# Optimization experiments

Measured on AMD Instinct MI355X. Metric: run time of the kernel, lower is better.

The kernel has to match this reference:

```python
import jax, jax.numpy as jnp
import numpy as np

B, T, D, H, HS = 2, 256, 2048, 32, 64
LORA, DLORA, ST = 32, 64, 66  # maa lora rank, decay lora rank, state rows (2+HS)
EPS = 1e-5


def setup_inputs() -> dict:
    key = jax.random.key(0)
    ks = jax.random.split(key, 24)
    n = lambda k, sh, s=0.02: (jax.random.normal(k, sh, jnp.float32) * s)
    u = lambda k, sh: jax.random.uniform(k, sh, jnp.float32)
    return {
        "x": jax.random.normal(ks[0], (B, T, D), jnp.float32),
        "state": jax.random.normal(ks[1], (B, ST, D), jnp.float32) * 0.1,
        "ln1_w": jnp.ones((D,), jnp.float32),
        "ln1_b": jnp.zeros((D,), jnp.float32),
        "time_maa_x": u(ks[2], (D,)),
        "time_maa_w1": n(ks[3], (D, 5 * LORA)),
        "time_maa_w2": n(ks[4], (5, LORA, D)),
        "time_maa_k": u(ks[5], (D,)),
        "time_maa_w": u(ks[6], (D,)),
        "time_maa_v": u(ks[7], (D,)),
        "time_maa_r": u(ks[8], (D,)),
        "time_maa_g": u(ks[9], (D,)),
        "time_decay": n(ks[10], (D,), 0.5),
        "time_decay_w1": n(ks[11], (D, DLORA)),
        "time_decay_w2": n(ks[12], (DLORA, D)),
        "time_faaaa": n(ks[13], (H, HS, 1), 0.1),
        "receptance_weight": n(ks[14], (D, D)),
        "key_weight": n(ks[15], (D, D)),
        "value_weight": n(ks[16], (D, D)),
        "output_weight": n(ks[17], (D, D)),
        "gate_weight": n(ks[18], (D, D)),
        "lnx_w": jnp.ones((D,), jnp.float32),
        "lnx_b": jnp.zeros((D,), jnp.float32),
        "i": 0,
    }


def reference(x, state, ln1_w, ln1_b, time_maa_x, time_maa_w1, time_maa_w2,
              time_maa_k, time_maa_w, time_maa_v, time_maa_r, time_maa_g,
              time_decay, time_decay_w1, time_decay_w2, time_faaaa,
              receptance_weight, key_weight, value_weight, output_weight,
              gate_weight, lnx_w, lnx_b, i):
    # forward() early-returns time_mixing(ln1(x), state, i)
    mu = x.mean(-1, keepdims=True)
    var = ((x - mu) ** 2).mean(-1, keepdims=True)
    x = (x - mu) * jax.lax.rsqrt(var + EPS) * ln1_w + ln1_b

    i1 = (2 + HS) * i + 1
    # token shift: sx[t] = x[t-1] - x[t], with state row i1 as x[-1]
    sx = jnp.concatenate([state[:, i1][:, None] - x[:, :1], x[:, :-1] - x[:, 1:]], axis=1)

    xxx = x + sx * time_maa_x
    t5 = jnp.tanh(xxx @ time_maa_w1).reshape(B, T, 5, LORA)
    xxx5 = jnp.einsum('btfr,frd->btfd', t5, time_maa_w2)          # [B,T,5,D]
    maa = jnp.stack([time_maa_k, time_maa_w, time_maa_v, time_maa_r, time_maa_g])  # [5,D]
    x5 = x[:, :, None] + sx[:, :, None] * (maa + xxx5)            # [B,T,5,D]

    k = (x5[:, :, 0] @ key_weight.T).reshape(B, T, H, HS)
    w = jnp.exp(-jnp.exp(time_decay + jnp.tanh(x5[:, :, 1] @ time_decay_w1) @ time_decay_w2)).reshape(B, T, H, HS)
    v = (x5[:, :, 2] @ value_weight.T).reshape(B, T, H, HS)
    r = (x5[:, :, 3] @ receptance_weight.T).reshape(B, T, H, HS)
    g = jax.nn.silu(x5[:, :, 4] @ gate_weight.T)                  # [B,T,D]

    kv = jnp.einsum('bthi,bthj->bthij', k, v)                     # [B,T,H,HS,HS]
    prev0 = state[:, i1 + 1:i1 + 1 + HS].reshape(B, H, HS, HS)

    def step(prev, xs):
        kv_t, w_t = xs
        return kv_t + w_t[..., None] * prev, prev  # emit state BEFORE update

    _, state_s = jax.lax.scan(step, prev0,
                              (kv.transpose(1, 0, 2, 3, 4), w.transpose(1, 0, 2, 3)))
    state_s = state_s.transpose(1, 0, 2, 3, 4)                    # [B,T,H,HS,HS]

    wkv = time_faaaa * kv + state_s
    rwkv = jnp.einsum('bthj,bthjd->bthd', r, wkv)                 # [B,T,H,HS]

    # GroupNorm(num_groups=H) over each head's HS channels
    gm = rwkv.mean(-1, keepdims=True)
    gv = ((rwkv - gm) ** 2).mean(-1, keepdims=True)
    normed = (rwkv - gm) * jax.lax.rsqrt(gv + EPS)
    normed = normed * lnx_w.reshape(H, HS) + lnx_b.reshape(H, HS)
    normed = normed.reshape(B, T, D)

    return (normed * g) @ output_weight.T
```

## Files before the change

kernel.cpp:

```cpp
#include <hip/hip_runtime.h>
#include <hip/hip_bf16.h>

typedef unsigned short u16;
typedef __attribute__((ext_vector_type(4))) float f32x4;
typedef __attribute__((ext_vector_type(8))) short short8;
typedef __attribute__((ext_vector_type(4))) short bf16x4;

#define B_ 2
#define T_ 256
#define D_ 2048
#define H_ 32
#define HS_ 64
#define M_ 512
#define ST_ 66
#define EPS_ 1e-5f
#define NC_ 16
#define CL_ 16

__device__ __forceinline__ float bf2f(u16 u) {
    union { unsigned int i; float f; } c; c.i = ((unsigned int)u) << 16; return c.f;
}
__device__ __forceinline__ u16 f2bf(float f) {
    union { unsigned int i; float f; } c; c.f = f;
    unsigned int r = c.i + 0x7fffu + ((c.i >> 16) & 1u);
    return (u16)(r >> 16);
}

__device__ __forceinline__ void gld16(const u16* g, u16* l) {
    __builtin_amdgcn_global_load_lds((const __attribute__((address_space(1))) void*)g,
                                     (__attribute__((address_space(3))) void*)l, 16, 0, 0);
}

__global__ __launch_bounds__(256) void wcvt_kernel(const float* __restrict__ wk, const float* __restrict__ wv,
                                                   const float* __restrict__ wr, const float* __restrict__ wg,
                                                   const float* __restrict__ wo, u16* __restrict__ out)
{
    const int wsel = blockIdx.y;
    const float* in = (wsel == 0) ? wk : (wsel == 1) ? wv : (wsel == 2) ? wr : (wsel == 3) ? wg : wo;
    const size_t e = ((size_t)blockIdx.x * 256 + threadIdx.x) * 8;
    f32x4 a = *(const f32x4*)(in + e);
    f32x4 b = *(const f32x4*)(in + e + 4);
    short8 o;
#pragma unroll
    for (int i = 0; i < 4; i++) { o[i] = (short)f2bf(a[i]); o[i + 4] = (short)f2bf(b[i]); }
    *(short8*)(out + (size_t)wsel * D_ * D_ + e) = o;
}

__global__ __launch_bounds__(256) void ln_kernel(const float* __restrict__ x, const float* __restrict__ w,
                                                 const float* __restrict__ bias, float* __restrict__ xln)
{
    const int row = blockIdx.x;
    const float* xr = x + (size_t)row * D_;
    float* orow = xln + (size_t)row * D_;
    const int t = threadIdx.x;
    f32x4 a0 = *(const f32x4*)(xr + t * 8);
    f32x4 a1 = *(const f32x4*)(xr + t * 8 + 4);
    float s = 0.f, q = 0.f;
#pragma unroll
    for (int i = 0; i < 4; i++) { s += a0[i] + a1[i]; q += a0[i]*a0[i] + a1[i]*a1[i]; }
#pragma unroll
    for (int off = 1; off < 64; off <<= 1) { s += __shfl_xor(s, off, 64); q += __shfl_xor(q, off, 64); }
    __shared__ float ls[4], lq[4];
    const int wid = t >> 6, lane = t & 63;
    if (lane == 0) { ls[wid] = s; lq[wid] = q; }
    __syncthreads();
    s = ls[0] + ls[1] + ls[2] + ls[3];
    q = lq[0] + lq[1] + lq[2] + lq[3];
    const float mu = s * (1.f / D_);
    const float var = q * (1.f / D_) - mu * mu;
    const float rs = rsqrtf(var + EPS_);
#pragma unroll
    for (int i = 0; i < 8; i++) {
        int d = t * 8 + i;
        float f = (i < 4) ? a0[i] : a1[i - 4];
        orow[d] = (f - mu) * rs * w[d] + bias[d];
    }
}

__global__ __launch_bounds__(256) void shift_kernel(const float* __restrict__ xln, const float* __restrict__ state,
                                                    const float* __restrict__ maax, const int* __restrict__ ip,
                                                    float* __restrict__ sx, u16* __restrict__ xxxb)
{
    const size_t gid = (size_t)blockIdx.x * 256 + threadIdx.x;
    const size_t e = gid * 4;
    const int row = (int)(e >> 11);
    const int d = (int)(e & 2047);
    const int tt = row & (T_ - 1);
    const int b = row >> 8;
    const float* prev;
    if (tt == 0) prev = state + ((size_t)b * ST_ + (size_t)(66 * ip[0] + 1)) * D_ + d;
    else         prev = xln + e - D_;
    f32x4 p = *(const f32x4*)prev;
    f32x4 c = *(const f32x4*)(xln + e);
    f32x4 mx = *(const f32x4*)(maax + d);
    f32x4 sv;
    bf16x4 xv;
#pragma unroll
    for (int i = 0; i < 4; i++) { sv[i] = p[i] - c[i]; xv[i] = (short)f2bf(c[i] + sv[i] * mx[i]); }
    *(f32x4*)(sx + e) = sv;
    *(bf16x4*)(xxxb + e) = xv;
}

__global__ __launch_bounds__(256) void txp_kernel(const float* __restrict__ in, u16* __restrict__ out,
                                                  int K, int N)
{
    __shared__ float tile[32][33];
    const int k0 = blockIdx.x * 32, n0 = blockIdx.y * 32;
    const int c = threadIdx.x & 31, r8 = threadIdx.x >> 5;
#pragma unroll
    for (int i = 0; i < 4; i++) {
        int r = r8 + i * 8;
        tile[r][c] = in[(size_t)(k0 + r) * N + (n0 + c)];
    }
    __syncthreads();
#pragma unroll
    for (int i = 0; i < 4; i++) {
        int r = r8 + i * 8;
        out[(size_t)(n0 + r) * K + (k0 + c)] = f2bf(tile[c][r]);
    }
}

template<int NN, bool TANH>
__global__ __launch_bounds__(256) void gsmall_kernel(const u16* __restrict__ A, const u16* __restrict__ Wt,
                                                     float* __restrict__ C, int ldc)
{
    __shared__ u16 As[128 * 32];
    __shared__ u16 Ws[64 * 32];
    const int tid = threadIdx.x;
    const int m0 = blockIdx.y * 128, n0 = blockIdx.x * 64;
    const int lane = tid & 63, wid = tid >> 6;
    const int wm = (wid >> 1) * 64, wn = (wid & 1) * 32;

    f32x4 acc[4][2];
#pragma unroll
    for (int i = 0; i < 4; i++)
#pragma unroll
        for (int j = 0; j < 2; j++) { acc[i][j][0]=0.f; acc[i][j][1]=0.f; acc[i][j][2]=0.f; acc[i][j][3]=0.f; }

    const int rA = tid >> 2;
    const int kA = (tid & 3) * 8;
    const u16* gA0 = A + (size_t)(m0 + rA) * D_ + kA;
    const u16* gA1 = A + (size_t)(m0 + rA + 64) * D_ + kA;
    int wrow = n0 + rA; if (wrow >= NN) wrow = NN - 1;
    const u16* gW = Wt + (size_t)wrow * D_ + kA;
    u16* lA0 = As + tid * 8;
    u16* lA1 = As + (tid + 256) * 8;
    u16* lW  = Ws + tid * 8;
    const u16* pa = As + (size_t)(wm + (lane & 15)) * 32 + (lane >> 4) * 8;
    const u16* pb = Ws + (size_t)(wn + (lane & 15)) * 32 + (lane >> 4) * 8;

    short8 a0 = *(const short8*)gA0;
    short8 a1 = *(const short8*)gA1;
    short8 w0 = *(const short8*)gW;

    for (int kt = 0; kt < D_; kt += 32) {
        const int kt2 = (kt + 32) & (D_ - 1);
        short8 na0 = *(const short8*)(gA0 + kt2);
        short8 na1 = *(const short8*)(gA1 + kt2);
        short8 nw0 = *(const short8*)(gW + kt2);
        __syncthreads();
        *(short8*)lA0 = a0;
        *(short8*)lA1 = a1;
        *(short8*)lW  = w0;
        __syncthreads();
        short8 av[4], bv[2];
#pragma unroll
        for (int mi = 0; mi < 4; mi++) av[mi] = *(const short8*)(pa + mi * 16 * 32);
#pragma unroll
        for (int ni = 0; ni < 2; ni++) bv[ni] = *(const short8*)(pb + ni * 16 * 32);
#pragma unroll
        for (int mi = 0; mi < 4; mi++)
#pragma unroll
            for (int ni = 0; ni < 2; ni++)
                acc[mi][ni] = __builtin_amdgcn_mfma_f32_16x16x32_bf16(av[mi], bv[ni], acc[mi][ni], 0, 0, 0);
        a0 = na0; a1 = na1; w0 = nw0;
    }
    const int cr = wm + (lane >> 4) * 4;
    const int cc = wn + (lane & 15);
#pragma unroll
    for (int mi = 0; mi < 4; mi++)
#pragma unroll
        for (int ni = 0; ni < 2; ni++) {
            const int col = n0 + cc + ni * 16;
            if (col < NN) {
#pragma unroll
                for (int j = 0; j < 4; j++) {
                    float v = acc[mi][ni][j];
                    if (TANH) v = tanhf(v);
                    C[(size_t)(m0 + cr + mi * 16 + j) * ldc + col] = v;
                }
            }
        }
}

__global__ __launch_bounds__(256) void maa2_kernel(const float* __restrict__ t5, const float* __restrict__ w2,
                                                   const float* __restrict__ xln, const float* __restrict__ sxp,
                                                   const float* __restrict__ mk, const float* __restrict__ mw,
                                                   const float* __restrict__ mv, const float* __restrict__ mr,
                                                   const float* __restrict__ mg, u16* __restrict__ x5)
{
    const int gid = blockIdx.x * 256 + threadIdx.x;
    const int d = gid & (D_ - 1);
    const int f = (gid >> 11) % 5;
    const int mg4 = gid / (5 * D_);
    const float* maa = (f == 0) ? mk : (f == 1) ? mw : (f == 2) ? mv : (f == 3) ? mr : mg;
    const float mf = maa[d];
    const float* w2f = w2 + (size_t)f * 32 * D_ + d;
    const float* t5b = t5 + (size_t)mg4 * 4 * 160 + f * 32;
    float a0 = 0, a1 = 0, a2 = 0, a3 = 0;
#pragma unroll 8
    for (int r = 0; r < 32; r++) {
        float wv = w2f[(size_t)r * D_];
        a0 = fmaf(t5b[r], wv, a0);
        a1 = fmaf(t5b[160 + r], wv, a1);
        a2 = fmaf(t5b[320 + r], wv, a2);
        a3 = fmaf(t5b[480 + r], wv, a3);
    }
    const float accs[4] = {a0, a1, a2, a3};
    const size_t m0 = (size_t)mg4 * 4;
#pragma unroll
    for (int mm = 0; mm < 4; mm++) {
        size_t e = (m0 + mm) * D_ + d;
        x5[(size_t)f * M_ * D_ + e] = f2bf(xln[e] + sxp[e] * (mf + accs[mm]));
    }
}

__global__ __launch_bounds__(256) void decay2_kernel(const float* __restrict__ td, const float* __restrict__ dw2,
                                                     const float* __restrict__ tdec, float* __restrict__ wout)
{
    const int gid = blockIdx.x * 256 + threadIdx.x;
    const int d = gid & (D_ - 1);
    const int mg4 = gid >> 11;
    const float* wp = dw2 + d;
    const float* tb = td + (size_t)mg4 * 4 * 64;
    float a0 = 0, a1 = 0, a2 = 0, a3 = 0;
#pragma unroll 8
    for (int r = 0; r < 64; r++) {
        float wv = wp[(size_t)r * D_];
        a0 = fmaf(tb[r], wv, a0);
        a1 = fmaf(tb[64 + r], wv, a1);
        a2 = fmaf(tb[128 + r], wv, a2);
        a3 = fmaf(tb[192 + r], wv, a3);
    }
    const float base = tdec[d];
    const float accs[4] = {a0, a1, a2, a3};
#pragma unroll
    for (int mm = 0; mm < 4; mm++)
        wout[((size_t)mg4 * 4 + mm) * D_ + d] = expf(-expf(base + accs[mm]));
}

__device__ __forceinline__ void gemm2p_body(const u16* __restrict__ A, const u16* __restrict__ Wb,
                                            float* __restrict__ C, int m0, int n0, int k0, int KC)
{
    __shared__ u16 As[2][128 * 64];
    __shared__ u16 Bs[2][64 * 64];
    const int tid = threadIdx.x;
    const int lane = tid & 63;
    const int wvd = tid >> 6;
    const int wm = (wvd >> 1) * 64;
    const int wn = (wvd & 1) * 32;

    f32x4 acc[4][2];
#pragma unroll
    for (int i = 0; i < 4; i++)
#pragma unroll
        for (int j = 0; j < 2; j++) { acc[i][j][0]=0.f; acc[i][j][1]=0.f; acc[i][j][2]=0.f; acc[i][j][3]=0.f; }

    const int srow = tid >> 3;
    const int sw8  = (((tid & 7) ^ (srow & 7)) << 3);
    const u16* Ag = A + (size_t)(m0 + srow) * D_ + k0 + sw8;
    const u16* Wg = Wb + (size_t)(n0 + srow) * D_ + k0 + sw8;
    const int ldst = tid * 8;

    const int rsw = (lane & 7) << 3;
    const int colb = (lane >> 4) * 8;
    const int fr = lane & 15;

#define STAGE_(bb, kt)                                                            \
    {                                                                             \
        _Pragma("unroll")                                                         \
        for (int i = 0; i < 4; i++)                                               \
            gld16(Ag + (size_t)(i * 32) * D_ + (kt), &As[bb][i * 2048 + ldst]);   \
        _Pragma("unroll")                                                         \
        for (int i = 0; i < 2; i++)                                               \
            gld16(Wg + (size_t)(i * 32) * D_ + (kt), &Bs[bb][i * 2048 + ldst]);   \
    }

    STAGE_(0, 0);
    __syncthreads();
    int cur = 0;
    for (int kt = 0; kt < KC; kt += 64) {
        if (kt + 64 < KC) STAGE_(cur ^ 1, kt + 64);
#pragma unroll
        for (int kk = 0; kk < 64; kk += 32) {
            const int c = (kk + colb) ^ rsw;
            short8 av[4], bv[2];
#pragma unroll
            for (int mi = 0; mi < 4; mi++)
                av[mi] = *(const short8*)&As[cur][(wm + mi * 16 + fr) * 64 + c];
#pragma unroll
            for (int ni = 0; ni < 2; ni++)
                bv[ni] = *(const short8*)&Bs[cur][(wn + ni * 16 + fr) * 64 + c];
#pragma unroll
            for (int mi = 0; mi < 4; mi++)
#pragma unroll
                for (int ni = 0; ni < 2; ni++)
                    acc[mi][ni] = __builtin_amdgcn_mfma_f32_16x16x32_bf16(av[mi], bv[ni], acc[mi][ni], 0, 0, 0);
        }
        __syncthreads();
        cur ^= 1;
    }
#undef STAGE_
    const int cr = wm + (lane >> 4) * 4;
    const int cc = wn + fr;
#pragma unroll
    for (int mi = 0; mi < 4; mi++)
#pragma unroll
        for (int ni = 0; ni < 2; ni++)
#pragma unroll
            for (int j = 0; j < 4; j++)
                C[(size_t)(m0 + cr + mi * 16 + j) * D_ + (n0 + cc + ni * 16)] = acc[mi][ni][j];
}

__global__ __launch_bounds__(256) void gemm4g_kernel(const u16* __restrict__ x5, const u16* __restrict__ wcvt,
                                                     float* __restrict__ kvK, float* __restrict__ kvV,
                                                     float* __restrict__ kvR, float* __restrict__ kvG)
{
    const int s = blockIdx.z;
    const u16* A = x5 + (size_t)(s == 0 ? 0 : s + 1) * M_ * D_;
    const u16* W = wcvt + (size_t)s * D_ * D_;
    float* C = (s == 0) ? kvK : (s == 1) ? kvV : (s == 2) ? kvR : kvG;
    gemm2p_body(A, W, C, blockIdx.y * 128, blockIdx.x * 64, 0, D_);
}

__global__ __launch_bounds__(256) void gemm1g_kernel(const u16* __restrict__ y, const u16* __restrict__ wo,
                                                     float* __restrict__ out, float* __restrict__ p0,
                                                     float* __restrict__ p1, float* __restrict__ p2)
{
    const int ks = blockIdx.z;
    float* C = (ks == 0) ? out : (ks == 1) ? p0 : (ks == 2) ? p1 : p2;
    gemm2p_body(y, wo, C, blockIdx.y * 128, blockIdx.x * 64, ks * 512, 512);
}

__global__ __launch_bounds__(256) void add3_kernel(float* __restrict__ dst, const float* __restrict__ s0,
                                                   const float* __restrict__ s1, const float* __restrict__ s2)
{
    const size_t e = ((size_t)blockIdx.x * 256 + threadIdx.x) * 4;
    f32x4 d = *(const f32x4*)(dst + e);
    f32x4 a = *(const f32x4*)(s0 + e);
    f32x4 b = *(const f32x4*)(s1 + e);
    f32x4 c = *(const f32x4*)(s2 + e);
#pragma unroll
    for (int i = 0; i < 4; i++) d[i] += (a[i] + b[i]) + c[i];
    *(f32x4*)(dst + e) = d;
}

__global__ __launch_bounds__(512) void rec1_kernel(const float* __restrict__ rB, const float* __restrict__ kB,
                                                   const float* __restrict__ wB, const float* __restrict__ vB,
                                                   const float* __restrict__ fa, float* __restrict__ rwkv,
                                                   float* __restrict__ CS, float* __restrict__ RP,
                                                   float* __restrict__ PC)
{
    const int bx = blockIdx.x;
    const int c  = bx & (NC_ - 1);
    const int bh = bx >> 4;
    const int h = bh & 31, b = bh >> 5;
    const int tid = threadIdx.x;
    const int wv = tid >> 6, lane = tid & 63;
    const int wg = wv >> 2;
    const int jb = lane >> 3, dsub = lane & 7;
    const int jbase = jb * 8;
    const int d0 = wg * 32 + (wv & 3) * 8 + dsub;

    __shared__ float stage[4][CL_][64];
    __shared__ float p2[CL_][8][64];
    __shared__ float p1[CL_][8];
    __shared__ float rpS[CL_ * 64];

    float S[8], pv[8], faj[8];
#pragma unroll
    for (int q = 0; q < 8; q++) { S[q] = 0.f; pv[q] = 1.f; faj[q] = fa[h * 64 + jbase + q]; }

    const size_t base = ((size_t)b * T_ * H_ + h) * HS_;
    const int t0 = c * CL_;
    const int arr = wv & 3;
    const float* mysrc = (arr == 0) ? rB : (arr == 1) ? kB : (arr == 2) ? wB : vB;
    const int ts0 = wg * 8 + (lane >> 4);
    const int sch = (lane & 15) * 4;
    const bool p1w = (wv == 0 && dsub == 0);

#pragma unroll
    for (int p = 0; p < 2; p++) {
        f32x4 v = *(const f32x4*)(mysrc + base + (size_t)(t0 + ts0 + p * 4) * (H_ * HS_) + sch);
        *(f32x4*)&stage[arr][ts0 + p * 4][sch] = v;
    }
    __syncthreads();

    f32x4 r0 = *(const f32x4*)&stage[0][0][jbase];
    f32x4 r1 = *(const f32x4*)&stage[0][0][jbase + 4];
    f32x4 k0 = *(const f32x4*)&stage[1][0][jbase];
    f32x4 k1 = *(const f32x4*)&stage[1][0][jbase + 4];
    f32x4 w0 = *(const f32x4*)&stage[2][0][jbase];
    f32x4 w1 = *(const f32x4*)&stage[2][0][jbase + 4];
    float vd = stage[3][0][d0];
#pragma unroll
    for (int ts = 0; ts < CL_; ++ts) {
        f32x4 nr0 = r0, nr1 = r1, nk0 = k0, nk1 = k1, nw0 = w0, nw1 = w1;
        float nvd = vd;
        if (ts + 1 < CL_) {
            nr0 = *(const f32x4*)&stage[0][ts + 1][jbase];
            nr1 = *(const f32x4*)&stage[0][ts + 1][jbase + 4];
            nk0 = *(const f32x4*)&stage[1][ts + 1][jbase];
            nk1 = *(const f32x4*)&stage[1][ts + 1][jbase + 4];
            nw0 = *(const f32x4*)&stage[2][ts + 1][jbase];
            nw1 = *(const f32x4*)&stage[2][ts + 1][jbase + 4];
            nvd = stage[3][ts + 1][d0];
        }
        float s1 = 0.f, s2 = 0.f;
#pragma unroll
        for (int q = 0; q < 4; q++) {
            s1 = fmaf(r0[q] * faj[q],     k0[q], s1);
            s1 = fmaf(r1[q] * faj[q + 4], k1[q], s1);
            s2 = fmaf(r0[q], S[q],     s2);
            s2 = fmaf(r1[q], S[q + 4], s2);
        }
        p2[ts][jb][d0 ^ (jb << 3)] = s2;
        if (p1w) {
            p1[ts][jb] = s1;
#pragma unroll
            for (int q = 0; q < 4; q++) {
                rpS[ts * 64 + jbase + q]     = r0[q] * pv[q];
                rpS[ts * 64 + jbase + 4 + q] = r1[q] * pv[q + 4];
            }
        }
#pragma unroll
        for (int q = 0; q < 4; q++) {
            pv[q]     *= w0[q];
            pv[q + 4] *= w1[q];
            S[q]       = fmaf(w0[q], S[q],     k0[q] * vd);
            S[q + 4]   = fmaf(w1[q], S[q + 4], k1[q] * vd);
        }
        r0 = nr0; r1 = nr1; k0 = nk0; k1 = nk1; w0 = nw0; w1 = nw1; vd = nvd;
    }
    __syncthreads();
#pragma unroll
    for (int p = 0; p < 2; p++) {
        const int ts = wv * 2 + p;
        f32x4 p1a = *(const f32x4*)&p1[ts][0];
        f32x4 p1b = *(const f32x4*)&p1[ts][4];
        float s1t = ((p1a[0] + p1a[1]) + (p1a[2] + p1a[3])) +
                    ((p1b[0] + p1b[1]) + (p1b[2] + p1b[3]));
        float s2t = 0.f;
#pragma unroll
        for (int j = 0; j < 8; j++) s2t += p2[ts][j][lane ^ (j << 3)];
        const float vvv = stage[3][ts][lane];
        rwkv[base + (size_t)(t0 + ts) * (H_ * HS_) + lane] = fmaf(vvv, s1t, s2t);
    }
    RP[(size_t)bx * (CL_ * 64) + tid]       = rpS[tid];
    RP[(size_t)bx * (CL_ * 64) + 512 + tid] = rpS[512 + tid];
#pragma unroll
    for (int q = 0; q < 8; q++)
        CS[(size_t)bx * 4096 + (size_t)(jbase + q) * 64 + d0] = S[q];
    if (p1w) {
#pragma unroll
        for (int q = 0; q < 8; q++)
            PC[(size_t)bx * 64 + jbase + q] = pv[q];
    }
}

__global__ __launch_bounds__(512) void rec2_kernel(const float* __restrict__ state, const int* __restrict__ ip,
                                                   float* __restrict__ CS, const float* __restrict__ PC)
{
    const int bh = blockIdx.x;
    const int b = bh >> 5, h = bh & 31;
    const int tid = threadIdx.x;
    const int o = tid * 8;
    const int jrow = tid >> 3;
    const float* Sp = state + (size_t)b * ST_ * D_ + (size_t)(66 * ip[0] + 2) * D_ + (size_t)h * HS_ * HS_;
    f32x4 c0 = *(const f32x4*)(Sp + o);
    f32x4 c1 = *(const f32x4*)(Sp + o + 4);
    for (int c = 0; c < NC_; ++c) {
        float* cs = CS + ((size_t)(bh * NC_ + c)) * 4096 + o;
        f32x4 l0 = *(const f32x4*)cs;
        f32x4 l1 = *(const f32x4*)(cs + 4);
        const float pc = PC[(size_t)(bh * NC_ + c) * 64 + jrow];
        f32x4 n0, n1;
#pragma unroll
        for (int i = 0; i < 4; i++) { n0[i] = fmaf(pc, c0[i], l0[i]); n1[i] = fmaf(pc, c1[i], l1[i]); }
        *(f32x4*)cs = c0;
        *(f32x4*)(cs + 4) = c1;
        c0 = n0; c1 = n1;
    }
}

__global__ __launch_bounds__(256) void rec3_kernel(const float* __restrict__ CS, const float* __restrict__ RP,
                                                   float* __restrict__ rwkv)
{
    const int bx = blockIdx.x;
    const int c  = bx & (NC_ - 1);
    const int bh = bx >> 4;
    const int h = bh & 31, b = bh >> 5;
    const int tid = threadIdx.x;
    __shared__ float Ss[4096];
    __shared__ float rp[CL_ * 64];
#pragma unroll
    for (int i = 0; i < 4; i++)
        *(f32x4*)&Ss[tid * 4 + i * 1024] = *(const f32x4*)(CS + (size_t)bx * 4096 + tid * 4 + i * 1024);
    *(f32x4*)&rp[tid * 4] = *(const f32x4*)(RP + (size_t)bx * (CL_ * 64) + tid * 4);
    __syncthreads();
    const int tl = tid >> 4;
    const int d4 = (tid & 15) * 4;
    f32x4 acc; acc[0] = acc[1] = acc[2] = acc[3] = 0.f;
    const float* rpr = &rp[tl * 64];
#pragma unroll 16
    for (int j = 0; j < 64; ++j) {
        const float rv = rpr[j];
        const f32x4 sv = *(const f32x4*)&Ss[j * 64 + d4];
#pragma unroll
        for (int i = 0; i < 4; i++) acc[i] = fmaf(rv, sv[i], acc[i]);
    }
    const size_t base = ((size_t)b * T_ * H_ + h) * HS_;
    float* o = rwkv + base + (size_t)(c * CL_ + tl) * (H_ * HS_) + d4;
    f32x4 cur = *(const f32x4*)o;
#pragma unroll
    for (int i = 0; i < 4; i++) cur[i] += acc[i];
    *(f32x4*)o = cur;
}

__global__ __launch_bounds__(256) void gn_kernel(const float* __restrict__ rwkv, const float* __restrict__ gpre,
                                                 const float* __restrict__ lnxw, const float* __restrict__ lnxb,
                                                 u16* __restrict__ y)
{
    const int g = blockIdx.x * 4 + (threadIdx.x >> 6);
    const int lane = threadIdx.x & 63;
    const size_t e = (size_t)g * 64 + lane;
    const float val = rwkv[e];
    float s = val, q = val * val;
#pragma unroll
    for (int off = 1; off < 64; off <<= 1) { s += __shfl_xor(s, off, 64); q += __shfl_xor(q, off, 64); }
    const float mu = s * (1.f / 64.f);
    const float var = q * (1.f / 64.f) - mu * mu;
    const float rs = rsqrtf(var + EPS_);
    const int hj = (int)(e & (size_t)(D_ - 1));
    const float nrm = (val - mu) * rs * lnxw[hj] + lnxb[hj];
    const float gp = gpre[e];
    const float gv = gp / (1.f + expf(-gp));
    y[e] = f2bf(nrm * gv);
}

extern "C" void kernel_launch(void* const* d_in, const int* in_sizes, int n_in,
                              void* d_out, int out_size, void* d_ws, size_t ws_size,
                              hipStream_t stream)
{
    const float* x     = (const float*)d_in[0];
    const float* state = (const float*)d_in[1];
    const float* ln1w  = (const float*)d_in[2];
    const float* ln1b  = (const float*)d_in[3];
    const float* maax  = (const float*)d_in[4];
    const float* w1    = (const float*)d_in[5];
    const float* w2    = (const float*)d_in[6];
    const float* maak  = (const float*)d_in[7];
    const float* maaw  = (const float*)d_in[8];
    const float* maav  = (const float*)d_in[9];
    const float* maar  = (const float*)d_in[10];
    const float* maag  = (const float*)d_in[11];
    const float* tdec  = (const float*)d_in[12];
    const float* dw1   = (const float*)d_in[13];
    const float* dw2   = (const float*)d_in[14];
    const float* fa    = (const float*)d_in[15];
    const float* wrec  = (const float*)d_in[16];
    const float* wkey  = (const float*)d_in[17];
    const float* wval  = (const float*)d_in[18];
    const float* wout  = (const float*)d_in[19];
    const float* wgate = (const float*)d_in[20];
    const float* lnxw  = (const float*)d_in[21];
    const float* lnxb  = (const float*)d_in[22];
    const int*   ip    = (const int*)d_in[23];

    char* ws = (char*)d_ws;
    const size_t MD = (size_t)M_ * D_;
    u16*   wcvt = (u16*)  (ws);
    float* xln  = (float*)(ws + ((size_t)40 << 20));
    float* sx   = (float*)(ws + ((size_t)44 << 20));
    u16*   xxxb = (u16*)  (ws + ((size_t)48 << 20));
    u16*   w1t  = (u16*)  (ws + ((size_t)50 << 20));
    u16*   dw1t = (u16*)  (ws + ((size_t)51 << 20));
    float* t5   = (float*)(ws + ((size_t)52 << 20));
    float* td   = (float*)(ws + ((size_t)53 << 20));
    u16*   x5   = (u16*)  (ws + ((size_t)54 << 20));
    float* wdec = (float*)(ws + ((size_t)64 << 20));
    float* kvK  = (float*)(ws + ((size_t)40 << 20));
    float* kvV  = (float*)(ws + ((size_t)44 << 20));
    float* kvR  = (float*)(ws + ((size_t)48 << 20));
    float* kvG  = (float*)(ws + ((size_t)68 << 20));
    float* rwkv = (float*)(ws + ((size_t)72 << 20));
    u16*   y    = (u16*)  (ws + ((size_t)76 << 20));
    float* CS   = (float*)(ws);
    float* RP   = (float*)(ws + ((size_t)16 << 20));
    float* PC   = (float*)(ws + ((size_t)20 << 20));
    float* pp0  = (float*)(ws + ((size_t)54 << 20));
    float* pp1  = (float*)(ws + ((size_t)58 << 20));
    float* pp2  = (float*)(ws + ((size_t)62 << 20));
    float* out  = (float*)d_out;

    hipLaunchKernelGGL(wcvt_kernel,   dim3(2048, 5),  dim3(256), 0, stream, wkey, wval, wrec, wgate, wout, wcvt);
    hipLaunchKernelGGL(ln_kernel,     dim3(512),      dim3(256), 0, stream, x, ln1w, ln1b, xln);
    hipLaunchKernelGGL(shift_kernel,  dim3(1024),     dim3(256), 0, stream, xln, state, maax, ip, sx, xxxb);
    hipLaunchKernelGGL(txp_kernel,    dim3(64, 5),    dim3(256), 0, stream, w1, w1t, D_, 160);
    hipLaunchKernelGGL(txp_kernel,    dim3(64, 2),    dim3(256), 0, stream, dw1, dw1t, D_, 64);
    hipLaunchKernelGGL((gsmall_kernel<160, true>), dim3(3, 4), dim3(256), 0, stream, xxxb, w1t, t5, 160);
    hipLaunchKernelGGL(maa2_kernel,   dim3(5120),     dim3(256), 0, stream, t5, w2, xln, sx, maak, maaw, maav, maar, maag, x5);
    hipLaunchKernelGGL((gsmall_kernel<64, true>),  dim3(1, 4), dim3(256), 0, stream, x5 + MD, dw1t, td, 64);
    hipLaunchKernelGGL(decay2_kernel, dim3(1024),     dim3(256), 0, stream, td, dw2, tdec, wdec);
    hipLaunchKernelGGL(gemm4g_kernel, dim3(32, 4, 4), dim3(256), 0, stream, x5, wcvt, kvK, kvV, kvR, kvG);
    hipLaunchKernelGGL(rec1_kernel,   dim3(B_ * H_ * NC_), dim3(512), 0, stream, kvR, kvK, wdec, kvV, fa, rwkv, CS, RP, PC);
    hipLaunchKernelGGL(rec2_kernel,   dim3(B_ * H_),  dim3(512), 0, stream, state, ip, CS, PC);
    hipLaunchKernelGGL(rec3_kernel,   dim3(B_ * H_ * NC_), dim3(256), 0, stream, CS, RP, rwkv);
    hipLaunchKernelGGL(gn_kernel,     dim3(4096),     dim3(256), 0, stream, rwkv, kvG, lnxw, lnxb, y);
    hipLaunchKernelGGL(gemm1g_kernel, dim3(32, 4, 4), dim3(256), 0, stream, y, wcvt + (size_t)4 * D_ * D_, out, pp0, pp1, pp2);
    hipLaunchKernelGGL(add3_kernel,   dim3(1024),     dim3(256), 0, stream, out, pp0, pp1, pp2);

    (void)in_sizes; (void)n_in; (void)out_size; (void)ws_size;
}
```

Baseline: 206.4 us.

## Replace low-occupancy MFMA small GEMMs with one-wave-per-output dot kernels

The two LoRA down-projection GEMMs (512x160 and 512x64, K=2048) were launched on only 12 and 4 blocks, leaving most compute units idle. They are replaced by a kernel that assigns one wavefront to each output element. Each lane does bf16 FMAs over a strided slice of K, followed by a shuffle reduction and an optional tanh. This buys far more parallelism at the cost of re-reading each A row once per output column, which adds a lot of cache traffic and drops the MFMA units.

```diff
diff --git a/kernel.cpp b/kernel.cpp
--- a/kernel.cpp
+++ b/kernel.cpp
@@ -120,77 +120,27 @@
     }
 }
 
-template<int NN, bool TANH>
-__global__ __launch_bounds__(256) void gsmall_kernel(const u16* __restrict__ A, const u16* __restrict__ Wt,
-                                                     float* __restrict__ C, int ldc)
-{
-    __shared__ u16 As[128 * 32];
-    __shared__ u16 Ws[64 * 32];
-    const int tid = threadIdx.x;
-    const int m0 = blockIdx.y * 128, n0 = blockIdx.x * 64;
-    const int lane = tid & 63, wid = tid >> 6;
-    const int wm = (wid >> 1) * 64, wn = (wid & 1) * 32;
-
-    f32x4 acc[4][2];
-#pragma unroll
-    for (int i = 0; i < 4; i++)
-#pragma unroll
-        for (int j = 0; j < 2; j++) { acc[i][j][0]=0.f; acc[i][j][1]=0.f; acc[i][j][2]=0.f; acc[i][j][3]=0.f; }
-
-    const int rA = tid >> 2;
-    const int kA = (tid & 3) * 8;
-    const u16* gA0 = A + (size_t)(m0 + rA) * D_ + kA;
-    const u16* gA1 = A + (size_t)(m0 + rA + 64) * D_ + kA;
-    int wrow = n0 + rA; if (wrow >= NN) wrow = NN - 1;
-    const u16* gW = Wt + (size_t)wrow * D_ + kA;
-    u16* lA0 = As + tid * 8;
-    u16* lA1 = As + (tid + 256) * 8;
-    u16* lW  = Ws + tid * 8;
-    const u16* pa = As + (size_t)(wm + (lane & 15)) * 32 + (lane >> 4) * 8;
-    const u16* pb = Ws + (size_t)(wn + (lane & 15)) * 32 + (lane >> 4) * 8;
-
-    short8 a0 = *(const short8*)gA0;
-    short8 a1 = *(const short8*)gA1;
-    short8 w0 = *(const short8*)gW;
-
-    for (int kt = 0; kt < D_; kt += 32) {
-        const int kt2 = (kt + 32) & (D_ - 1);
-        short8 na0 = *(const short8*)(gA0 + kt2);
-        short8 na1 = *(const short8*)(gA1 + kt2);
-        short8 nw0 = *(const short8*)(gW + kt2);
-        __syncthreads();
-        *(short8*)lA0 = a0;
-        *(short8*)lA1 = a1;
-        *(short8*)lW  = w0;
-        __syncthreads();
-        short8 av[4], bv[2];
-#pragma unroll
-        for (int mi = 0; mi < 4; mi++) av[mi] = *(const short8*)(pa + mi * 16 * 32);
-#pragma unroll
-        for (int ni = 0; ni < 2; ni++) bv[ni] = *(const short8*)(pb + ni * 16 * 32);
-#pragma unroll
-        for (int mi = 0; mi < 4; mi++)
-#pragma unroll
-            for (int ni = 0; ni < 2; ni++)
-                acc[mi][ni] = __builtin_amdgcn_mfma_f32_16x16x32_bf16(av[mi], bv[ni], acc[mi][ni], 0, 0, 0);
-        a0 = na0; a1 = na1; w0 = nw0;
-    }
-    const int cr = wm + (lane >> 4) * 4;
-    const int cc = wn + (lane & 15);
-#pragma unroll
-    for (int mi = 0; mi < 4; mi++)
-#pragma unroll
-        for (int ni = 0; ni < 2; ni++) {
-            const int col = n0 + cc + ni * 16;
-            if (col < NN) {
-#pragma unroll
-                for (int j = 0; j < 4; j++) {
-                    float v = acc[mi][ni][j];
-                    if (TANH) v = tanhf(v);
-                    C[(size_t)(m0 + cr + mi * 16 + j) * ldc + col] = v;
-                }
-            }
-        }
+template<bool TANH>
+__global__ __launch_bounds__(512) void wdot_kernel(const u16* __restrict__ A, const u16* __restrict__ Wt,
+                                                   float* __restrict__ C, int N)
+{
+    const int gw = (int)((blockIdx.x * 512 + threadIdx.x) >> 6);
+    const int lane = threadIdx.x & 63;
+    const int m = gw / N, n = gw - m * N;
+    const u16* a = A + (size_t)m * D_ + lane * 8;
+    const u16* w = Wt + (size_t)n * D_ + lane * 8;
+    float acc = 0.f;
+#pragma unroll
+    for (int i = 0; i < 4; i++) {
+        short8 av = *(const short8*)(a + i * 512);
+        short8 wv = *(const short8*)(w + i * 512);
+#pragma unroll
+        for (int j = 0; j < 8; j++)
+            acc = fmaf(bf2f((u16)av[j]), bf2f((u16)wv[j]), acc);
+    }
+#pragma unroll
+    for (int off = 1; off < 64; off <<= 1) acc += __shfl_xor(acc, off, 64);
+    if (lane == 0) C[gw] = TANH ? tanhf(acc) : acc;
 }
 
 __global__ __launch_bounds__(256) void maa2_kernel(const float* __restrict__ t5, const float* __restrict__ w2,
@@ -608,9 +558,9 @@
     hipLaunchKernelGGL(shift_kernel,  dim3(1024),     dim3(256), 0, stream, xln, state, maax, ip, sx, xxxb);
     hipLaunchKernelGGL(txp_kernel,    dim3(64, 5),    dim3(256), 0, stream, w1, w1t, D_, 160);
     hipLaunchKernelGGL(txp_kernel,    dim3(64, 2),    dim3(256), 0, stream, dw1, dw1t, D_, 64);
-    hipLaunchKernelGGL((gsmall_kernel<160, true>), dim3(3, 4), dim3(256), 0, stream, xxxb, w1t, t5, 160);
+    hipLaunchKernelGGL((wdot_kernel<true>), dim3(10240), dim3(512), 0, stream, xxxb, w1t, t5, 160);
     hipLaunchKernelGGL(maa2_kernel,   dim3(5120),     dim3(256), 0, stream, t5, w2, xln, sx, maak, maaw, maav, maar, maag, x5);
-    hipLaunchKernelGGL((gsmall_kernel<64, true>),  dim3(1, 4), dim3(256), 0, stream, x5 + MD, dw1t, td, 64);
+    hipLaunchKernelGGL((wdot_kernel<true>), dim3(4096), dim3(512), 0, stream, x5 + MD, dw1t, td, 64);
     hipLaunchKernelGGL(decay2_kernel, dim3(1024),     dim3(256), 0, stream, td, dw2, tdec, wdec);
     hipLaunchKernelGGL(gemm4g_kernel, dim3(32, 4, 4), dim3(256), 0, stream, x5, wcvt, kvK, kvV, kvR, kvG);
     hipLaunchKernelGGL(rec1_kernel,   dim3(B_ * H_ * NC_), dim3(512), 0, stream, kvR, kvK, wdec, kvV, fa, rwkv, CS, RP, PC);
```

Result: faster. 197.4 us (-4.3%).
